# Optimization experiments

Measured on AMD Instinct MI355X. Metric: run time of the kernel, lower is better.

The kernel has to match this reference:

```python
import jax, jax.numpy as jnp
import numpy as np
from jax import lax

N_NODES = 20000
N_EDGES = 320000
FEAT = 100
N_RULES = 64
T_RULE = 50
H_RNN = 256
RULE_NUMS = 16
NTN_OUT = 200


def setup_inputs() -> dict:
    key = jax.random.key(0)
    ks = iter(jax.random.split(key, 64))
    nrm = lambda shape, s=0.05: jax.random.normal(next(ks), shape, jnp.float32) * s
    inp = {}
    inp["node_features_0"] = jax.random.normal(next(ks), (N_NODES, FEAT), jnp.float32)
    inp["node_features_1"] = jax.random.normal(next(ks), (N_NODES, FEAT), jnp.float32)
    inp["edge_indices_0"] = jax.random.randint(next(ks), (2, N_EDGES), 0, N_NODES)
    inp["edge_indices_1"] = jax.random.randint(next(ks), (2, N_EDGES), 0, N_NODES)
    inp["edge_features_0"] = jax.random.normal(next(ks), (N_EDGES, FEAT), jnp.float32)
    inp["edge_features_1"] = jax.random.normal(next(ks), (N_EDGES, FEAT), jnp.float32)
    inp["rules"] = jax.random.normal(next(ks), (N_RULES, T_RULE, FEAT), jnp.float32)
    # TripleConv 1: edge lin (3*100 -> 100) and nn = mlp (100->100->100)
    inp["c1_lin_W"] = nrm((FEAT, 3 * FEAT)); inp["c1_lin_b"] = jnp.zeros((FEAT,))
    inp["c1_W1"] = nrm((FEAT, FEAT)); inp["c1_b1"] = jnp.zeros((FEAT,))
    inp["c1_W2"] = nrm((FEAT, FEAT)); inp["c1_b2"] = jnp.zeros((FEAT,))
    # TripleConv 2
    inp["c2_lin_W"] = nrm((FEAT, 3 * FEAT)); inp["c2_lin_b"] = jnp.zeros((FEAT,))
    inp["c2_W1"] = nrm((FEAT, FEAT)); inp["c2_b1"] = jnp.zeros((FEAT,))
    inp["c2_W2"] = nrm((FEAT, FEAT)); inp["c2_b2"] = jnp.zeros((FEAT,))
    # NTN (input_dim=100 to match pooled graph vectors, out_dim=200)
    inp["ntn_W"] = nrm((FEAT, FEAT, NTN_OUT))
    inp["ntn_V"] = nrm((NTN_OUT, 2 * FEAT))
    inp["ntn_B"] = jnp.zeros((NTN_OUT,))
    # RuleEmbedding: 2-layer tanh RNN (100 -> 256 -> 256) + Linear(256,100)
    inp["rnn0_Wih"] = nrm((H_RNN, FEAT)); inp["rnn0_Whh"] = nrm((H_RNN, H_RNN))
    inp["rnn0_bih"] = jnp.zeros((H_RNN,)); inp["rnn0_bhh"] = jnp.zeros((H_RNN,))
    inp["rnn1_Wih"] = nrm((H_RNN, H_RNN)); inp["rnn1_Whh"] = nrm((H_RNN, H_RNN))
    inp["rnn1_bih"] = jnp.zeros((H_RNN,)); inp["rnn1_bhh"] = jnp.zeros((H_RNN,))
    inp["rule_lin_W"] = nrm((FEAT, H_RNN)); inp["rule_lin_b"] = jnp.zeros((FEAT,))
    # RuleRanker 100->128->64->1
    inp["rk_W1"] = nrm((128, FEAT)); inp["rk_b1"] = jnp.zeros((128,))
    inp["rk_W2"] = nrm((64, 128)); inp["rk_b2"] = jnp.zeros((64,))
    inp["rk_W3"] = nrm((1, 64)); inp["rk_b3"] = jnp.zeros((1,))
    # Head: fc1 (200 + rule_nums*100 -> 500) -> fc2 (500->100) -> fc3 (100->1)
    inp["fc1_W"] = nrm((500, NTN_OUT + RULE_NUMS * FEAT)); inp["fc1_b"] = jnp.zeros((500,))
    inp["fc2_W"] = nrm((FEAT, 500)); inp["fc2_b"] = jnp.zeros((FEAT,))
    inp["fc3_W"] = nrm((1, FEAT)); inp["fc3_b"] = jnp.zeros((1,))
    return inp


def _triple_conv(x, src, dst, e, lin_W, lin_b, W1, b1, W2, b2):
    # message: relu(Linear(concat(x_i, edge_attr, x_j))); PyG: i=target, j=source
    m = jax.nn.relu(jnp.concatenate([x[dst], e, x[src]], axis=1) @ lin_W.T + lin_b)
    agg = jax.ops.segment_sum(m, dst, num_segments=x.shape[0])  # aggr='add'
    out = agg + x  # (1 + eps) * x_r with eps = 0
    h = jax.nn.relu(out @ W1.T + b1)
    return h @ W2.T + b2  # nn = Sequential(Linear, ReLU, Linear)


def _conv_pass(x, ei, e, c_lin_W, c_lin_b, c_W1, c_b1, c_W2, c_b2,
               d_lin_W, d_lin_b, d_W1, d_b1, d_W2, d_b2):
    src, dst = ei[0], ei[1]
    x = jax.nn.relu(_triple_conv(x, src, dst, e, c_lin_W, c_lin_b, c_W1, c_b1, c_W2, c_b2))
    x = jax.nn.relu(_triple_conv(x, src, dst, e, d_lin_W, d_lin_b, d_W1, d_b1, d_W2, d_b2))
    return x


def _rnn_layer(x_tbf, Wih, Whh, bih, bhh):
    # x_tbf: [T, B, in]; returns all hidden states [T, B, H] and final [B, H]
    h0 = jnp.zeros((x_tbf.shape[1], Whh.shape[0]), x_tbf.dtype)
    def step(h, xt):
        h = jnp.tanh(xt @ Wih.T + bih + h @ Whh.T + bhh)
        return h, h
    hT, ys = lax.scan(step, h0, x_tbf)
    return ys, hT


def reference(node_features_0, node_features_1, edge_indices_0, edge_indices_1,
              edge_features_0, edge_features_1, rules,
              c1_lin_W, c1_lin_b, c1_W1, c1_b1, c1_W2, c1_b2,
              c2_lin_W, c2_lin_b, c2_W1, c2_b1, c2_W2, c2_b2,
              ntn_W, ntn_V, ntn_B,
              rnn0_Wih, rnn0_Whh, rnn0_bih, rnn0_bhh,
              rnn1_Wih, rnn1_Whh, rnn1_bih, rnn1_bhh,
              rule_lin_W, rule_lin_b,
              rk_W1, rk_b1, rk_W2, rk_b2, rk_W3, rk_b3,
              fc1_W, fc1_b, fc2_W, fc2_b, fc3_W, fc3_b):
    # --- rule embedding (all sequences full length => pack/pad is identity) ---
    x = jnp.transpose(rules, (1, 0, 2))  # [T, B, 100]
    ys, _ = _rnn_layer(x, rnn0_Wih, rnn0_Whh, rnn0_bih, rnn0_bhh)
    _, hT = _rnn_layer(ys, rnn1_Wih, rnn1_Whh, rnn1_bih, rnn1_bhh)
    rules_embedding = hT @ rule_lin_W.T + rule_lin_b  # [B, 100]
    # --- rule ranking + top-k ---
    h = jax.nn.relu(rules_embedding @ rk_W1.T + rk_b1)
    h = jax.nn.relu(h @ rk_W2.T + rk_b2)
    rules_score = jax.nn.sigmoid(h @ rk_W3.T + rk_b3)[:, 0]  # [B]
    _, top_idx = lax.top_k(rules_score, RULE_NUMS)
    top_rules_embedding = rules_embedding[top_idx]  # [rule_nums, 100]
    # --- GNN message passing on both graphs ---
    f1 = _conv_pass(node_features_0, edge_indices_0, edge_features_0,
                    c1_lin_W, c1_lin_b, c1_W1, c1_b1, c1_W2, c1_b2,
                    c2_lin_W, c2_lin_b, c2_W1, c2_b1, c2_W2, c2_b2)
    f2 = _conv_pass(node_features_1, edge_indices_1, edge_features_1,
                    c1_lin_W, c1_lin_b, c1_W1, c1_b1, c1_W2, c1_b2,
                    c2_lin_W, c2_lin_b, c2_W1, c2_b1, c2_W2, c2_b2)
    g1 = jnp.sum(f1, axis=0, keepdims=True)  # global_add_pool, single graph -> [1, 100]
    g2 = jnp.sum(f2, axis=0, keepdims=True)
    # --- NTN(g1, g2) ---
    tp = jnp.einsum('ai,ijk,bj->abk', g1, ntn_W, g2)  # [1,1,200]
    concat = jnp.concatenate([g1[:, None, :] * jnp.ones_like(g2)[None, :, :1],
                              g2[None, :, :] * jnp.ones_like(g1)[:, None, :1]], axis=2)
    lin_term = concat @ ntn_V.T  # [1,1,200]
    ntn_out = jax.nn.relu(tp + lin_term + ntn_B).reshape(-1)  # squeeze -> [200]
    # --- scoring head ---
    feat = jnp.concatenate([ntn_out, top_rules_embedding.reshape(-1)])  # [200 + rule_nums*100]
    z = jax.nn.relu(feat @ fc1_W.T + fc1_b)
    z = jax.nn.relu(z @ fc2_W.T + fc2_b)
    score = jax.nn.sigmoid(z @ fc3_W.T + fc3_b)
    return score.reshape(())
```

## Files before the change

### kernel.cpp

```cpp
#include <hip/hip_runtime.h>

typedef unsigned short u16;
typedef unsigned int u32;

#define N_NODES 20000
#define N_EDGES 320000
#define FEAT 100
#define XPAD 112
#define MPAD 104
#define N_RULES 64
#define T_RULE 50
#define H_RNN 256
#define RULE_NUMS 16
#define NTN_OUT 200
#define SCAN_B 79

typedef __attribute__((ext_vector_type(8))) short short8;
typedef __attribute__((ext_vector_type(4))) float f32x4;

__device__ __forceinline__ u16 f2bu(float f) {
  u32 u = __float_as_uint(f);
  u32 r = (u + 0x7fffu + ((u >> 16) & 1u)) >> 16;
  return (u16)r;
}
__device__ __forceinline__ float bu2f(u16 u) {
  return __uint_as_float(((u32)u) << 16);
}
__device__ __forceinline__ u32 pk2(float a, float b) {
  return (u32)f2bu(a) | ((u32)f2bu(b) << 16);
}

__device__ __forceinline__ void lds_st16(void* base, int byteOff, uint4 v) {
  *(uint4*)((char*)base + byteOff) = v;
}
__device__ __forceinline__ short8 lds_ld16(const void* base, int byteOff) {
  return *(const short8*)((const char*)base + byteOff);
}

#define SWZ(row, kByte) (((((row) << 8) + (kByte))) ^ (((row) & 7) << 4))

__device__ __forceinline__ int hs_off(int row, int chunk) {
  return (row << 9) | (((chunk + row * 5) & 31) << 4);
}

__device__ __forceinline__ float tanh_fast(float x) {
  const float e = __expf(2.f * x);
  return 1.f - 2.f / (e + 1.f);
}

__global__ void k_prep(const float* __restrict__ nf0, const float* __restrict__ nf1,
                       u16* __restrict__ xb0, u16* __restrict__ xb1) {
  const int total = N_NODES * XPAD;
  for (int i = blockIdx.x * blockDim.x + threadIdx.x; i < total;
       i += gridDim.x * blockDim.x) {
    const int n = i / XPAD;
    const int c = i - n * XPAD;
    const float v0 = (c < FEAT) ? nf0[(size_t)n * FEAT + c] : 0.f;
    const float v1 = (c < FEAT) ? nf1[(size_t)n * FEAT + c] : 0.f;
    xb0[i] = f2bu(v0);
    xb1[i] = f2bu(v1);
  }
}

__global__ void k_wprep(const float* __restrict__ linW, u16* __restrict__ Wb) {
  const int idx = blockIdx.x * blockDim.x + threadIdx.x;
  if (idx >= 3 * 128 * 128) return;
  const int c = idx >> 14;
  const int rem = idx & 16383;
  const int r = rem >> 7;
  const int k = rem & 127;
  u16 v = 0;
  if (r < FEAT && k < FEAT) v = f2bu(linW[(size_t)r * 300 + c * 100 + k]);
  Wb[idx] = v;
}

__global__ void k_wprep_sq(const float* __restrict__ W, u16* __restrict__ Wb) {
  const int idx = blockIdx.x * blockDim.x + threadIdx.x;
  if (idx >= 128 * 128) return;
  const int r = idx >> 7;
  const int k = idx & 127;
  u16 v = 0;
  if (r < FEAT && k < FEAT) v = f2bu(W[(size_t)r * FEAT + k]);
  Wb[idx] = v;
}

__global__ void k_count2(const int* __restrict__ d0, const int* __restrict__ d1,
                         int* __restrict__ cnt) {
  const int e = blockIdx.x * blockDim.x + threadIdx.x;
  const int* d = blockIdx.y ? d1 : d0;
  if (e < N_EDGES) atomicAdd(&cnt[blockIdx.y * N_NODES + d[e]], 1);
}

__global__ __launch_bounds__(256) void k_scan1(const int* __restrict__ cnt,
                                               int* __restrict__ off,
                                               int* __restrict__ bsum) {
  __shared__ int buf[256];
  const int g = blockIdx.y, b = blockIdx.x, tid = threadIdx.x;
  const int i = b * 256 + tid;
  const int v = (i < N_NODES) ? cnt[g * N_NODES + i] : 0;
  buf[tid] = v;
  __syncthreads();
  for (int ofs = 1; ofs < 256; ofs <<= 1) {
    const int t = (tid >= ofs) ? buf[tid - ofs] : 0;
    __syncthreads();
    buf[tid] += t;
    __syncthreads();
  }
  if (i < N_NODES) off[g * (N_NODES + 1) + i] = buf[tid] - v;
  if (tid == 255) bsum[g * SCAN_B + b] = buf[255];
}

__global__ __launch_bounds__(128) void k_scan2(int* __restrict__ bsum) {
  __shared__ int s[128];
  const int g = blockIdx.y, tid = threadIdx.x;
  const int v = (tid < SCAN_B) ? bsum[g * SCAN_B + tid] : 0;
  s[tid] = v;
  __syncthreads();
  for (int ofs = 1; ofs < 128; ofs <<= 1) {
    const int t = (tid >= ofs) ? s[tid - ofs] : 0;
    __syncthreads();
    s[tid] += t;
    __syncthreads();
  }
  if (tid < SCAN_B) bsum[g * SCAN_B + tid] = s[tid] - v;
}

__global__ __launch_bounds__(256) void k_scan3(const int* __restrict__ bsum,
                                               int* __restrict__ off,
                                               int* __restrict__ cursor) {
  const int g = blockIdx.y, b = blockIdx.x, tid = threadIdx.x;
  const int i = b * 256 + tid;
  if (i < N_NODES) {
    const int o = off[g * (N_NODES + 1) + i] + bsum[g * SCAN_B + b];
    off[g * (N_NODES + 1) + i] = o;
    cursor[g * N_NODES + i] = o;
  }
  if (i == N_NODES) off[g * (N_NODES + 1) + N_NODES] = N_EDGES;
}

__global__ void k_scatter2(const int* __restrict__ d0, const int* __restrict__ d1,
                           int* __restrict__ cursor, int* __restrict__ rank0,
                           int* __restrict__ rank1) {
  const int e = blockIdx.x * blockDim.x + threadIdx.x;
  const int g = blockIdx.y;
  const int* d = g ? d1 : d0;
  if (e < N_EDGES) {
    const int pos = atomicAdd(&cursor[g * N_NODES + d[e]], 1);
    (g ? rank1 : rank0)[e] = pos;
  }
}

template <int VARIANT>
__global__ __launch_bounds__(256) void k_gemm_u(
    const float* __restrict__ Af, const u16* __restrict__ Ab,
    const float* __restrict__ W, const float* __restrict__ b0,
    const float* __restrict__ b1, float* __restrict__ Uout) {
  __shared__ __align__(16) u16 As[64 * 128];
  __shared__ __align__(16) u16 Bs[128 * 128];
  const int tid = threadIdx.x;
  const int lane = tid & 63;
  const int wv = tid >> 6;
  const int l15 = lane & 15;
  const int lhi = lane >> 4;
  const int mb = blockIdx.x * 64;
  const int nb = blockIdx.y * 128;
  const int rb = (wv >> 1) * 32;
  const int cb = (wv & 1) * 64;
  constexpr int KV = VARIANT ? 256 : 100;
  constexpr int NPH = VARIANT ? 2 : 1;

  f32x4 acc[2][4];
  const f32x4 z4 = {0.f, 0.f, 0.f, 0.f};
#pragma unroll
  for (int i = 0; i < 2; ++i)
#pragma unroll
    for (int j = 0; j < 4; ++j) acc[i][j] = z4;

  for (int kc = 0; kc < NPH; ++kc) {
    __syncthreads();
    {
      const int row = tid >> 2;
      const int k0 = (tid & 3) * 32;
      const int gm = mb + row;
      if (VARIANT == 0) {
        const int r = gm & 63;
        const int t = gm >> 6;
        const float* ar = Af + ((size_t)r * T_RULE + t) * FEAT;
#pragma unroll
        for (int c = 0; c < 4; ++c) {
          const int k = k0 + c * 8;
          uint4 v = {0u, 0u, 0u, 0u};
          if (k + 8 <= KV) {
            const float4 fa = *(const float4*)(ar + k);
            const float4 fb = *(const float4*)(ar + k + 4);
            v.x = pk2(fa.x, fa.y); v.y = pk2(fa.z, fa.w);
            v.z = pk2(fb.x, fb.y); v.w = pk2(fb.z, fb.w);
          } else if (k < KV) {
            const float4 fa = *(const float4*)(ar + k);
            v.x = pk2(fa.x, fa.y); v.y = pk2(fa.z, fa.w);
          }
          lds_st16(As, SWZ(row, k * 2), v);
        }
      } else {
        const uint4* ar = (const uint4*)(Ab + (size_t)gm * 256 + kc * 128 + k0);
#pragma unroll
        for (int c = 0; c < 4; ++c)
          lds_st16(As, SWZ(row, (k0 + c * 8) * 2), ar[c]);
      }
    }
    {
      const int row = tid >> 1;
      const int k0 = (tid & 1) * 64;
      const float* wr = W + (size_t)(nb + row) * KV;
#pragma unroll
      for (int c = 0; c < 8; ++c) {
        const int k = k0 + c * 8;
        const int kg = kc * 128 + k;
        uint4 v = {0u, 0u, 0u, 0u};
        if (kg + 8 <= KV) {
          const float4 fa = *(const float4*)(wr + kg);
          const float4 fb = *(const float4*)(wr + kg + 4);
          v.x = pk2(fa.x, fa.y); v.y = pk2(fa.z, fa.w);
          v.z = pk2(fb.x, fb.y); v.w = pk2(fb.z, fb.w);
        } else if (kg < KV) {
          const float4 fa = *(const float4*)(wr + kg);
          v.x = pk2(fa.x, fa.y); v.y = pk2(fa.z, fa.w);
        }
        lds_st16(Bs, SWZ(row, k * 2), v);
      }
    }
    __syncthreads();
#pragma unroll
    for (int s = 0; s < 4; ++s) {
      const int kByte = s * 64 + lhi * 16;
      short8 af[2], bfr[4];
#pragma unroll
      for (int i = 0; i < 2; ++i)
        af[i] = lds_ld16(As, SWZ(rb + i * 16 + l15, kByte));
#pragma unroll
      for (int j = 0; j < 4; ++j)
        bfr[j] = lds_ld16(Bs, SWZ(cb + j * 16 + l15, kByte));
#pragma unroll
      for (int i = 0; i < 2; ++i)
#pragma unroll
        for (int j = 0; j < 4; ++j)
          acc[i][j] = __builtin_amdgcn_mfma_f32_16x16x32_bf16(af[i], bfr[j],
                                                              acc[i][j], 0, 0, 0);
    }
  }
#pragma unroll
  for (int j = 0; j < 4; ++j) {
    const int col = nb + cb + j * 16 + l15;
    const float bias = b0[col] + b1[col];
#pragma unroll
    for (int i = 0; i < 2; ++i) {
      const int base_m = mb + rb + i * 16 + lhi * 4;
      const int t = base_m >> 6;
      const int r0 = base_m & 63;
      float4 st;
      st.x = acc[i][j][0] + bias; st.y = acc[i][j][1] + bias;
      st.z = acc[i][j][2] + bias; st.w = acc[i][j][3] + bias;
      *(float4*)(Uout + ((size_t)t * 256 + col) * 64 + r0) = st;
    }
  }
}

template <int WRITE_YS>
__global__ __launch_bounds__(512) void k_rec(
    const float* __restrict__ U, const float* __restrict__ Whh,
    u16* __restrict__ ys, float* __restrict__ hT) {
  __shared__ __align__(16) u16 Hs[16 * 256];
  const int tid = threadIdx.x;
  const int lane = tid & 63;
  const int wv = tid >> 6;
  const int cbase = wv * 32;
  const int ruleBase = blockIdx.x * 16;
  const int l15 = lane & 15;
  const int lhi = lane >> 4;

  short8 bf[2][8];
#pragma unroll
  for (int jt = 0; jt < 2; ++jt) {
    const int col = cbase + jt * 16 + l15;
    const float* wr = Whh + (size_t)col * 256;
#pragma unroll
    for (int s = 0; s < 8; ++s) {
      const int k0 = s * 32 + lhi * 8;
      const float4 fa = *(const float4*)(wr + k0);
      const float4 fb = *(const float4*)(wr + k0 + 4);
      uint4 v;
      v.x = pk2(fa.x, fa.y); v.y = pk2(fa.z, fa.w);
      v.z = pk2(fb.x, fb.y); v.w = pk2(fb.z, fb.w);
      bf[jt][s] = *(short8*)&v;
    }
  }
  for (int i = tid; i < 16 * 256 / 8; i += 512) {
    const uint4 z = {0u, 0u, 0u, 0u};
    ((uint4*)Hs)[i] = z;
  }
  __syncthreads();

  const int n0 = cbase + l15;
  const int n1 = cbase + 16 + l15;
  const int m0 = lhi * 4;
  float4 Ua0 = *(const float4*)(U + ((size_t)n0) * 64 + m0);
  float4 Ua1 = *(const float4*)(U + ((size_t)n1) * 64 + m0);

  const f32x4 z4 = {0.f, 0.f, 0.f, 0.f};
  float hv[2][4];
  for (int t = 0; t < T_RULE; ++t) {
    const int tn = (t + 1 < T_RULE) ? t + 1 : t;
    const float4 Ub0 = *(const float4*)(U + ((size_t)tn * 256 + n0) * 64 + m0);
    const float4 Ub1 = *(const float4*)(U + ((size_t)tn * 256 + n1) * 64 + m0);
    f32x4 acc[2] = {z4, z4};
#pragma unroll
    for (int s = 0; s < 8; ++s) {
      const short8 af = lds_ld16(Hs, hs_off(l15, s * 4 + lhi));
      acc[0] = __builtin_amdgcn_mfma_f32_16x16x32_bf16(af, bf[0][s], acc[0], 0, 0, 0);
      acc[1] = __builtin_amdgcn_mfma_f32_16x16x32_bf16(af, bf[1][s], acc[1], 0, 0, 0);
    }
    const float ua0[4] = {Ua0.x, Ua0.y, Ua0.z, Ua0.w};
    const float ua1[4] = {Ua1.x, Ua1.y, Ua1.z, Ua1.w};
#pragma unroll
    for (int q = 0; q < 4; ++q) {
      hv[0][q] = tanh_fast(ua0[q] + acc[0][q]);
      hv[1][q] = tanh_fast(ua1[q] + acc[1][q]);
    }
    __syncthreads();
#pragma unroll
    for (int jt = 0; jt < 2; ++jt) {
      const int n = cbase + jt * 16 + l15;
#pragma unroll
      for (int q = 0; q < 4; ++q) {
        const int m = lhi * 4 + q;
        const u16 hb = f2bu(hv[jt][q]);
        *(u16*)((char*)Hs + (hs_off(m, n >> 3) + ((n & 7) << 1))) = hb;
        if (WRITE_YS)
          ys[(((size_t)t * 64 + ruleBase + m) << 8) + n] = hb;
      }
    }
    Ua0 = Ub0; Ua1 = Ub1;
    __syncthreads();
  }
  if (!WRITE_YS) {
#pragma unroll
    for (int jt = 0; jt < 2; ++jt) {
      const int n = cbase + jt * 16 + l15;
#pragma unroll
      for (int q = 0; q < 4; ++q) {
        const int m = lhi * 4 + q;
        hT[((size_t)(ruleBase + m) << 8) + n] = hv[jt][q];
      }
    }
  }
}

__global__ __launch_bounds__(128) void k_rulelin(
    const float* __restrict__ hT, const float* __restrict__ rlW,
    const float* __restrict__ rlb, float* __restrict__ emb) {
  __shared__ __align__(16) float hs[H_RNN];
  const int b = blockIdx.x;
  const int tid = threadIdx.x;
  for (int i = tid; i < H_RNN / 4; i += 128)
    ((float4*)hs)[i] = ((const float4*)(hT + (size_t)b * H_RNN))[i];
  __syncthreads();
  if (tid < FEAT) {
    float acc = rlb[tid];
    const float4* w = (const float4*)(rlW + (size_t)tid * H_RNN);
    const float4* hv = (const float4*)hs;
#pragma unroll 8
    for (int k = 0; k < 64; ++k) {
      const float4 a = w[k], x = hv[k];
      acc += a.x * x.x + a.y * x.y + a.z * x.z + a.w * x.w;
    }
    emb[(size_t)b * FEAT + tid] = acc;
  }
}

__global__ __launch_bounds__(128) void k_ranker(
    const float* __restrict__ emb,
    const float* __restrict__ W1, const float* __restrict__ b1,
    const float* __restrict__ W2, const float* __restrict__ b2,
    const float* __restrict__ W3, const float* __restrict__ b3,
    float* __restrict__ scores) {
  __shared__ float eb[FEAT];
  __shared__ float h1s[128];
  __shared__ float h2s[64];
  const int r = blockIdx.x;
  const int tid = threadIdx.x;
  if (tid < FEAT) eb[tid] = emb[(size_t)r * FEAT + tid];
  __syncthreads();
  {
    float acc = b1[tid];
    const float* w = W1 + (size_t)tid * FEAT;
    for (int k = 0; k < FEAT; ++k) acc += w[k] * eb[k];
    h1s[tid] = acc > 0.f ? acc : 0.f;
  }
  __syncthreads();
  if (tid < 64) {
    float acc = b2[tid];
    const float* w = W2 + (size_t)tid * 128;
    for (int k = 0; k < 128; ++k) acc += w[k] * h1s[k];
    h2s[tid] = acc > 0.f ? acc : 0.f;
  }
  __syncthreads();
  if (tid == 0) {
    float acc = b3[0];
    for (int k = 0; k < 64; ++k) acc += W3[k] * h2s[k];
    scores[r] = acc;
  }
}

__global__ void k_topk(const float* __restrict__ scores, int* __restrict__ topidx) {
  if (threadIdx.x == 0 && blockIdx.x == 0) {
    float s[N_RULES];
    for (int i = 0; i < N_RULES; ++i) s[i] = scores[i];
    for (int t = 0; t < RULE_NUMS; ++t) {
      int best = 0;
      float bv = s[0];
      for (int i = 1; i < N_RULES; ++i)
        if (s[i] > bv) { bv = s[i]; best = i; }
      topidx[t] = best;
      s[best] = -1e30f;
    }
  }
}

__global__ __launch_bounds__(256) void k_nodegemm(
    const u16* __restrict__ xb, const u16* __restrict__ Wb,
    const float* __restrict__ linB, u16* __restrict__ P, u16* __restrict__ Q) {
  __shared__ __align__(16) u16 As[128 * 128];
  __shared__ __align__(16) u16 Bs[128 * 128];
  const int tid = threadIdx.x;
  const int lane = tid & 63;
  const int wv = tid >> 6;
  const int l15 = lane & 15;
  const int lhi = lane >> 4;
  const int n0 = blockIdx.x * 128;
  const int p = blockIdx.y;
  const int rStage = tid >> 1;
  const int hf = tid & 1;
  const int rb = (wv >> 1) * 64;
  const int cb = (wv & 1) * 64;

  {
    const int node = n0 + rStage;
    const bool ok = node < N_NODES;
    const uint4* xr = (const uint4*)(xb + (size_t)node * XPAD);
#pragma unroll
    for (int q = 0; q < 8; ++q) {
      const int cc = hf * 8 + q;
      uint4 v = {0u, 0u, 0u, 0u};
      if (ok && cc < 14) v = xr[cc];
      lds_st16(As, SWZ(rStage, cc * 16), v);
    }
  }
  {
    const uint4* wr = (const uint4*)(Wb + (size_t)(p ? 2 : 0) * 16384 +
                                     (size_t)rStage * 128);
#pragma unroll
    for (int q = 0; q < 8; ++q) {
      const int cc = hf * 8 + q;
      lds_st16(Bs, SWZ(rStage, cc * 16), wr[cc]);
    }
  }
  __syncthreads();

  f32x4 acc[4][4];
  const f32x4 z4 = {0.f, 0.f, 0.f, 0.f};
#pragma unroll
  for (int i = 0; i < 4; ++i)
#pragma unroll
    for (int j = 0; j < 4; ++j) acc[i][j] = z4;
#pragma unroll
  for (int s = 0; s < 4; ++s) {
    const int kByte = s * 64 + lhi * 16;
    short8 af[4], bfr[4];
#pragma unroll
    for (int i = 0; i < 4; ++i) {
      af[i] = lds_ld16(As, SWZ(rb + i * 16 + l15, kByte));
      bfr[i] = lds_ld16(Bs, SWZ(cb + i * 16 + l15, kByte));
    }
#pragma unroll
    for (int i = 0; i < 4; ++i)
#pragma unroll
      for (int j = 0; j < 4; ++j)
        acc[i][j] = __builtin_amdgcn_mfma_f32_16x16x32_bf16(af[i], bfr[j],
                                                            acc[i][j], 0, 0, 0);
  }
  u16* Out = p ? Q : P;
#pragma unroll
  for (int j = 0; j < 4; ++j) {
    const int col = cb + j * 16 + l15;
    if (col >= XPAD) continue;
    const bool valid = col < FEAT;
    const float bias = (valid && !p) ? linB[col] : 0.f;
#pragma unroll
    for (int i = 0; i < 4; ++i) {
      const int row0 = rb + i * 16 + lhi * 4;
#pragma unroll
      for (int q = 0; q < 4; ++q) {
        const int node = n0 + row0 + q;
        if (node < N_NODES)
          Out[(size_t)node * XPAD + col] = valid ? f2bu(acc[i][j][q] + bias) : (u16)0;
      }
    }
  }
}

__global__ __launch_bounds__(256) void k_msgE(
    const float* __restrict__ ef, const u16* __restrict__ Wb,
    const int* __restrict__ srcI, const int* __restrict__ dstI,
    const int* __restrict__ rank, const u16* __restrict__ Pb,
    const u16* __restrict__ Qb, u16* __restrict__ mOut) {
  __shared__ __align__(16) u16 As[64 * 128];
  __shared__ __align__(16) u16 Bs[128 * 128];
  const int tid = threadIdx.x;
  const int lane = tid & 63;
  const int wv = tid >> 6;
  const int l15 = lane & 15;
  const int lhi = lane >> 4;
  const int e0 = blockIdx.x * 64;

  const int rr = tid >> 2;
  const int t4 = tid & 3;
  const int ge = e0 + rr;
  const int dn = dstI[ge];
  const int sn = srcI[ge];
  const int rk = rank[ge];
  uint4 pv[4], qv[4];
#pragma unroll
  for (int c = 0; c < 4; ++c) {
    const int chunk = t4 * 4 + c;
    uint4 z = {0u, 0u, 0u, 0u};
    pv[c] = z; qv[c] = z;
    if (chunk < 14) {
      pv[c] = *(const uint4*)(Pb + (size_t)dn * XPAD + chunk * 8);
      qv[c] = *(const uint4*)(Qb + (size_t)sn * XPAD + chunk * 8);
    }
  }

  {
    const int row = tid >> 2;
    const int k0 = (tid & 3) * 32;
    const float* ar = ef + (size_t)(e0 + row) * FEAT;
#pragma unroll
    for (int c = 0; c < 4; ++c) {
      const int k = k0 + c * 8;
      uint4 v = {0u, 0u, 0u, 0u};
      if (k + 8 <= FEAT) {
        const float4 fa = *(const float4*)(ar + k);
        const float4 fb = *(const float4*)(ar + k + 4);
        v.x = pk2(fa.x, fa.y); v.y = pk2(fa.z, fa.w);
        v.z = pk2(fb.x, fb.y); v.w = pk2(fb.z, fb.w);
      } else if (k < FEAT) {
        const float4 fa = *(const float4*)(ar + k);
        v.x = pk2(fa.x, fa.y); v.y = pk2(fa.z, fa.w);
      }
      lds_st16(As, SWZ(row, k * 2), v);
    }
  }
  {
    const int row = tid >> 1;
    const int hf = tid & 1;
    const uint4* wr = (const uint4*)(Wb + 16384 + (size_t)row * 128);
#pragma unroll
    for (int q = 0; q < 8; ++q) {
      const int cc = hf * 8 + q;
      lds_st16(Bs, SWZ(row, cc * 16), wr[cc]);
    }
  }
  __syncthreads();

  const int rb = (wv >> 1) * 32;
  const int cb = (wv & 1) * 64;
  f32x4 acc[2][4];
  const f32x4 z4 = {0.f, 0.f, 0.f, 0.f};
#pragma unroll
  for (int i = 0; i < 2; ++i)
#pragma unroll
    for (int j = 0; j < 4; ++j) acc[i][j] = z4;
#pragma unroll
  for (int s = 0; s < 4; ++s) {
    const int kByte = s * 64 + lhi * 16;
    short8 af[2], bfr[4];
#pragma unroll
    for (int i = 0; i < 2; ++i)
      af[i] = lds_ld16(As, SWZ(rb + i * 16 + l15, kByte));
#pragma unroll
    for (int j = 0; j < 4; ++j)
      bfr[j] = lds_ld16(Bs, SWZ(cb + j * 16 + l15, kByte));
#pragma unroll
    for (int i = 0; i < 2; ++i)
#pragma unroll
      for (int j = 0; j < 4; ++j)
        acc[i][j] = __builtin_amdgcn_mfma_f32_16x16x32_bf16(af[i], bfr[j],
                                                            acc[i][j], 0, 0, 0);
  }
  __syncthreads();
#pragma unroll
  for (int i = 0; i < 2; ++i) {
#pragma unroll
    for (int j = 0; j < 4; ++j) {
      const int col = cb + j * 16 + l15;
#pragma unroll
      for (int q = 0; q < 4; ++q) {
        const int row = rb + i * 16 + lhi * 4 + q;
        *(u16*)((char*)As + (SWZ(row, col * 2))) = f2bu(acc[i][j][q]);
      }
    }
  }
  __syncthreads();
#pragma unroll
  for (int c = 0; c < 4; ++c) {
    const int chunk = t4 * 4 + c;
    if (chunk > 12) break;
    const short8 ev = lds_ld16(As, SWZ(rr, chunk * 16));
    const uint4 e4 = *(const uint4*)&ev;
    const uint4 p4 = pv[c];
    const uint4 q4 = qv[c];
    uint4 o;
    {
      float v0 = bu2f((u16)(e4.x & 0xffffu)) + bu2f((u16)(p4.x & 0xffffu)) +
                 bu2f((u16)(q4.x & 0xffffu));
      float v1 = bu2f((u16)(e4.x >> 16)) + bu2f((u16)(p4.x >> 16)) +
                 bu2f((u16)(q4.x >> 16));
      o.x = pk2(v0 > 0.f ? v0 : 0.f, v1 > 0.f ? v1 : 0.f);
      float v2 = bu2f((u16)(e4.y & 0xffffu)) + bu2f((u16)(p4.y & 0xffffu)) +
                 bu2f((u16)(q4.y & 0xffffu));
      float v3 = bu2f((u16)(e4.y >> 16)) + bu2f((u16)(p4.y >> 16)) +
                 bu2f((u16)(q4.y >> 16));
      o.y = pk2(v2 > 0.f ? v2 : 0.f, v3 > 0.f ? v3 : 0.f);
      float v4 = bu2f((u16)(e4.z & 0xffffu)) + bu2f((u16)(p4.z & 0xffffu)) +
                 bu2f((u16)(q4.z & 0xffffu));
      float v5 = bu2f((u16)(e4.z >> 16)) + bu2f((u16)(p4.z >> 16)) +
                 bu2f((u16)(q4.z >> 16));
      o.z = pk2(v4 > 0.f ? v4 : 0.f, v5 > 0.f ? v5 : 0.f);
      float v6 = bu2f((u16)(e4.w & 0xffffu)) + bu2f((u16)(p4.w & 0xffffu)) +
                 bu2f((u16)(q4.w & 0xffffu));
      float v7 = bu2f((u16)(e4.w >> 16)) + bu2f((u16)(p4.w >> 16)) +
                 bu2f((u16)(q4.w >> 16));
      o.w = pk2(v6 > 0.f ? v6 : 0.f, v7 > 0.f ? v7 : 0.f);
    }
    *(uint4*)(mOut + (size_t)rk * MPAD + chunk * 8) = o;
  }
}

__global__ __launch_bounds__(256) void k_agg(
    const u16* __restrict__ mPerm, const int* __restrict__ off,
    const u16* __restrict__ xb, u16* __restrict__ aggb) {
  const int tid = threadIdx.x;
  const int ln = tid >> 5;
  const int j = tid & 31;
  const int n = blockIdx.x * 8 + ln;
  if (j >= 28) return;
  u16* outp = aggb + (size_t)n * XPAD + j * 4;
  if (j >= 26) {
    uint2 z = {0u, 0u};
    *(uint2*)outp = z;
    return;
  }
  const int p0 = off[n], p1 = off[n + 1];
  float a0 = 0.f, a1 = 0.f, a2 = 0.f, a3 = 0.f;
  const u16* mp = mPerm + (size_t)j * 4;
  int p = p0;
  for (; p + 3 < p1; p += 4) {
    const uint2 u0 = *(const uint2*)(mp + (size_t)p * MPAD);
    const uint2 u1 = *(const uint2*)(mp + (size_t)(p + 1) * MPAD);
    const uint2 u2 = *(const uint2*)(mp + (size_t)(p + 2) * MPAD);
    const uint2 u3 = *(const uint2*)(mp + (size_t)(p + 3) * MPAD);
    a0 += bu2f((u16)(u0.x & 0xffffu)) + bu2f((u16)(u1.x & 0xffffu)) +
          bu2f((u16)(u2.x & 0xffffu)) + bu2f((u16)(u3.x & 0xffffu));
    a1 += bu2f((u16)(u0.x >> 16)) + bu2f((u16)(u1.x >> 16)) +
          bu2f((u16)(u2.x >> 16)) + bu2f((u16)(u3.x >> 16));
    a2 += bu2f((u16)(u0.y & 0xffffu)) + bu2f((u16)(u1.y & 0xffffu)) +
          bu2f((u16)(u2.y & 0xffffu)) + bu2f((u16)(u3.y & 0xffffu));
    a3 += bu2f((u16)(u0.y >> 16)) + bu2f((u16)(u1.y >> 16)) +
          bu2f((u16)(u2.y >> 16)) + bu2f((u16)(u3.y >> 16));
  }
  for (; p < p1; ++p) {
    const uint2 u0 = *(const uint2*)(mp + (size_t)p * MPAD);
    a0 += bu2f((u16)(u0.x & 0xffffu));
    a1 += bu2f((u16)(u0.x >> 16));
    a2 += bu2f((u16)(u0.y & 0xffffu));
    a3 += bu2f((u16)(u0.y >> 16));
  }
  const uint2 xv = *(const uint2*)(xb + (size_t)n * XPAD + j * 4);
  a0 += bu2f((u16)(xv.x & 0xffffu));
  a1 += bu2f((u16)(xv.x >> 16));
  a2 += bu2f((u16)(xv.y & 0xffffu));
  a3 += bu2f((u16)(xv.y >> 16));
  uint2 o;
  o.x = pk2(a0, a1);
  o.y = pk2(a2, a3);
  *(uint2*)outp = o;
}

__global__ __launch_bounds__(256) void k_mlp(
    const u16* __restrict__ aggb, const u16* __restrict__ W1b,
    const float* __restrict__ b1, const u16* __restrict__ W2b,
    const float* __restrict__ b2, u16* __restrict__ xbout) {
  __shared__ __align__(16) u16 As[128 * 128];
  __shared__ __align__(16) u16 Bs[128 * 128];
  const int tid = threadIdx.x;
  const int lane = tid & 63;
  const int wv = tid >> 6;
  const int l15 = lane & 15;
  const int lhi = lane >> 4;
  const int n0 = blockIdx.x * 128;
  const int rStage = tid >> 1;
  const int hf = tid & 1;
  const int rb = (wv >> 1) * 64;
  const int cb = (wv & 1) * 64;
  const f32x4 z4 = {0.f, 0.f, 0.f, 0.f};

  {
    const int node = n0 + rStage;
    const bool ok = node < N_NODES;
    const uint4* xr = (const uint4*)(aggb + (size_t)node * XPAD);
#pragma unroll
    for (int q = 0; q < 8; ++q) {
      const int cc = hf * 8 + q;
      uint4 v = {0u, 0u, 0u, 0u};
      if (ok && cc < 14) v = xr[cc];
      lds_st16(As, SWZ(rStage, cc * 16), v);
    }
  }
  {
    const uint4* wr = (const uint4*)(W1b + (size_t)rStage * 128);
#pragma unroll
    for (int q = 0; q < 8; ++q) {
      const int cc = hf * 8 + q;
      lds_st16(Bs, SWZ(rStage, cc * 16), wr[cc]);
    }
  }
  __syncthreads();

  f32x4 acc[4][4];
#pragma unroll
  for (int i = 0; i < 4; ++i)
#pragma unroll
    for (int j = 0; j < 4; ++j) acc[i][j] = z4;
#pragma unroll
  for (int s = 0; s < 4; ++s) {
    const int kByte = s * 64 + lhi * 16;
    short8 af[4], bfr[4];
#pragma unroll
    for (int i = 0; i < 4; ++i) {
      af[i] = lds_ld16(As, SWZ(rb + i * 16 + l15, kByte));
      bfr[i] = lds_ld16(Bs, SWZ(cb + i * 16 + l15, kByte));
    }
#pragma unroll
    for (int i = 0; i < 4; ++i)
#pragma unroll
      for (int j = 0; j < 4; ++j)
        acc[i][j] = __builtin_amdgcn_mfma_f32_16x16x32_bf16(af[i], bfr[j],
                                                            acc[i][j], 0, 0, 0);
  }
  __syncthreads();
#pragma unroll
  for (int j = 0; j < 4; ++j) {
    const int col = cb + j * 16 + l15;
    const float bias = (col < FEAT) ? b1[col] : 0.f;
#pragma unroll
    for (int i = 0; i < 4; ++i) {
      const int row0 = rb + i * 16 + lhi * 4;
#pragma unroll
      for (int q = 0; q < 4; ++q) {
        float v = acc[i][j][q] + bias;
        v = v > 0.f ? v : 0.f;
        *(u16*)((char*)As + (SWZ(row0 + q, col * 2))) = f2bu(v);
      }
    }
  }
  {
    const uint4* wr = (const uint4*)(W2b + (size_t)rStage * 128);
#pragma unroll
    for (int q = 0; q < 8; ++q) {
      const int cc = hf * 8 + q;
      lds_st16(Bs, SWZ(rStage, cc * 16), wr[cc]);
    }
  }
  __syncthreads();

#pragma unroll
  for (int i = 0; i < 4; ++i)
#pragma unroll
    for (int j = 0; j < 4; ++j) acc[i][j] = z4;
#pragma unroll
  for (int s = 0; s < 4; ++s) {
    const int kByte = s * 64 + lhi * 16;
    short8 af[4], bfr[4];
#pragma unroll
    for (int i = 0; i < 4; ++i) {
      af[i] = lds_ld16(As, SWZ(rb + i * 16 + l15, kByte));
      bfr[i] = lds_ld16(Bs, SWZ(cb + i * 16 + l15, kByte));
    }
#pragma unroll
    for (int i = 0; i < 4; ++i)
#pragma unroll
      for (int j = 0; j < 4; ++j)
        acc[i][j] = __builtin_amdgcn_mfma_f32_16x16x32_bf16(af[i], bfr[j],
                                                            acc[i][j], 0, 0, 0);
  }
#pragma unroll
  for (int j = 0; j < 4; ++j) {
    const int col = cb + j * 16 + l15;
    if (col >= XPAD) continue;
    const bool valid = col < FEAT;
    const float bias = valid ? b2[col] : 0.f;
#pragma unroll
    for (int i = 0; i < 4; ++i) {
      const int row0 = rb + i * 16 + lhi * 4;
#pragma unroll
      for (int q = 0; q < 4; ++q) {
        const int node = n0 + row0 + q;
        if (node < N_NODES) {
          float v = acc[i][j][q] + bias;
          v = v > 0.f ? v : 0.f;
          xbout[(size_t)node * XPAD + col] = valid ? f2bu(v) : (u16)0;
        }
      }
    }
  }
}

__global__ void k_pool(const u16* __restrict__ xb, float* __restrict__ g) {
  const int tid = threadIdx.x;
  if (tid >= FEAT) return;
  float s = 0.f;
  const int n0 = blockIdx.x * 100;
  for (int i = 0; i < 100; ++i) s += bu2f(xb[(size_t)(n0 + i) * XPAD + tid]);
  atomicAdd(&g[tid], s);
}

__global__ __launch_bounds__(256) void k_ntn(const float* __restrict__ W,
                                             const float* __restrict__ g1,
                                             const float* __restrict__ g2,
                                             float* __restrict__ tp) {
  __shared__ float g2s[FEAT];
  const int i = blockIdx.x;
  const int tid = threadIdx.x;
  if (tid < FEAT) g2s[tid] = g2[tid];
  __syncthreads();
  if (tid < NTN_OUT) {
    const float g1i = g1[i];
    float acc = 0.f;
    const float* wr = W + (size_t)i * FEAT * NTN_OUT + tid;
    for (int jj = 0; jj < FEAT; ++jj) acc += wr[(size_t)jj * NTN_OUT] * g2s[jj];
    atomicAdd(&tp[tid], g1i * acc);
  }
}

__global__ __launch_bounds__(256) void k_feat(
    const float* __restrict__ tp, const float* __restrict__ gv,
    const float* __restrict__ V, const float* __restrict__ B,
    const float* __restrict__ emb, const int* __restrict__ topidx,
    float* __restrict__ featOut) {
  const int tid = threadIdx.x;
  if (tid < NTN_OUT) {
    float acc = B[tid] + tp[tid];
    const float* vr = V + (size_t)tid * 200;
    for (int k = 0; k < 200; ++k) acc += vr[k] * gv[k];
    featOut[tid] = acc > 0.f ? acc : 0.f;
  }
  for (int i = tid; i < RULE_NUMS * FEAT; i += 256) {
    const int rr = i / FEAT;
    const int cc = i - rr * FEAT;
    featOut[NTN_OUT + i] = emb[(size_t)topidx[rr] * FEAT + cc];
  }
}

__global__ __launch_bounds__(256) void k_fc1(
    const float* __restrict__ feat, const float* __restrict__ W,
    const float* __restrict__ b, float* __restrict__ z1) {
  __shared__ __align__(16) float fs[NTN_OUT + RULE_NUMS * FEAT];
  const int tid = threadIdx.x;
  for (int i = tid; i < 450; i += 256) ((float4*)fs)[i] = ((const float4*)feat)[i];
  __syncthreads();
  const int lane = tid & 63;
  const int wv = tid >> 6;
  const int o = blockIdx.x * 4 + wv;
  float acc = 0.f;
  const float4* w4 = (const float4*)(W + (size_t)o * 1800);
  const float4* f4 = (const float4*)fs;
  for (int k = lane; k < 450; k += 64) {
    const float4 a = w4[k], x = f4[k];
    acc += a.x * x.x + a.y * x.y + a.z * x.z + a.w * x.w;
  }
#pragma unroll
  for (int d = 32; d; d >>= 1) acc += __shfl_down(acc, d);
  if (lane == 0) {
    acc += b[o];
    z1[o] = acc > 0.f ? acc : 0.f;
  }
}

__global__ __launch_bounds__(128) void k_head2(
    const float* __restrict__ z1g, const float* __restrict__ fc2W,
    const float* __restrict__ fc2b, const float* __restrict__ fc3W,
    const float* __restrict__ fc3b, float* __restrict__ out) {
  __shared__ __align__(16) float z1[500];
  __shared__ float z2[FEAT];
  const int tid = threadIdx.x;
  for (int i = tid; i < 125; i += 128) ((float4*)z1)[i] = ((const float4*)z1g)[i];
  __syncthreads();
  if (tid < FEAT) {
    float acc = fc2b[tid];
    const float4* w4 = (const float4*)(fc2W + (size_t)tid * 500);
    const float4* f4 = (const float4*)z1;
#pragma unroll 5
    for (int k = 0; k < 125; ++k) {
      const float4 a = w4[k], x = f4[k];
      acc += a.x * x.x + a.y * x.y + a.z * x.z + a.w * x.w;
    }
    z2[tid] = acc > 0.f ? acc : 0.f;
  }
  __syncthreads();
  if (tid == 0) {
    float acc = fc3b[0];
    for (int k = 0; k < FEAT; ++k) acc += fc3W[k] * z2[k];
    out[0] = 1.f / (1.f + expf(-acc));
  }
}

extern "C" void kernel_launch(void* const* d_in, const int* in_sizes, int n_in,
                              void* d_out, int out_size, void* d_ws, size_t ws_size,
                              hipStream_t stream) {
  (void)in_sizes; (void)n_in; (void)out_size; (void)ws_size;

  const float* nf[2] = {(const float*)d_in[0], (const float*)d_in[1]};
  const int* ei[2] = {(const int*)d_in[2], (const int*)d_in[3]};
  const float* ef[2] = {(const float*)d_in[4], (const float*)d_in[5]};
  const float* rules = (const float*)d_in[6];
  const float* cw[2][6];
  for (int l = 0; l < 2; ++l)
    for (int k = 0; k < 6; ++k) cw[l][k] = (const float*)d_in[7 + l * 6 + k];
  const float* ntnW = (const float*)d_in[19];
  const float* ntnV = (const float*)d_in[20];
  const float* ntnB = (const float*)d_in[21];
  const float* r0Wih = (const float*)d_in[22];
  const float* r0Whh = (const float*)d_in[23];
  const float* r0bih = (const float*)d_in[24];
  const float* r0bhh = (const float*)d_in[25];
  const float* r1Wih = (const float*)d_in[26];
  const float* r1Whh = (const float*)d_in[27];
  const float* r1bih = (const float*)d_in[28];
  const float* r1bhh = (const float*)d_in[29];
  const float* rlW = (const float*)d_in[30];
  const float* rlb = (const float*)d_in[31];
  const float* rkW1 = (const float*)d_in[32];
  const float* rkb1 = (const float*)d_in[33];
  const float* rkW2 = (const float*)d_in[34];
  const float* rkb2 = (const float*)d_in[35];
  const float* rkW3 = (const float*)d_in[36];
  const float* rkb3 = (const float*)d_in[37];
  const float* fc1W = (const float*)d_in[38];
  const float* fc1b = (const float*)d_in[39];
  const float* fc2W = (const float*)d_in[40];
  const float* fc2b = (const float*)d_in[41];
  const float* fc3W = (const float*)d_in[42];
  const float* fc3b = (const float*)d_in[43];

  char* base = (char*)d_ws;
  size_t woff = 0;
#define WS_ALLOC(T, NAME, BYTES) \
  T* NAME = (T*)(base + woff);   \
  woff = (woff + (size_t)(BYTES) + 255) & ~(size_t)255;
  WS_ALLOC(u16, m_buf, (size_t)N_EDGES * MPAD * 2)
  WS_ALLOC(u16, xb0, (size_t)N_NODES * XPAD * 2)
  WS_ALLOC(u16, xb1, (size_t)N_NODES * XPAD * 2)
  WS_ALLOC(u16, Pbuf, (size_t)N_NODES * XPAD * 2)
  WS_ALLOC(u16, Qbuf, (size_t)N_NODES * XPAD * 2)
  WS_ALLOC(u16, aggb, (size_t)N_NODES * XPAD * 2)
  WS_ALLOC(u16, Wb0, (size_t)3 * 128 * 128 * 2)
  WS_ALLOC(u16, Wb1, (size_t)3 * 128 * 128 * 2)
  WS_ALLOC(u16, Wm, (size_t)4 * 128 * 128 * 2)
  WS_ALLOC(int, offAll, (size_t)2 * (N_NODES + 1) * 4)
  WS_ALLOC(int, cursor, (size_t)2 * N_NODES * 4)
  WS_ALLOC(int, bsum, (size_t)2 * SCAN_B * 4)
  WS_ALLOC(int, rank0, (size_t)N_EDGES * 4)
  WS_ALLOC(int, rank1, (size_t)N_EDGES * 4)
  WS_ALLOC(float, emb, (size_t)N_RULES * FEAT * 4)
  WS_ALLOC(float, scores, (size_t)N_RULES * 4)
  WS_ALLOC(int, topidx, (size_t)RULE_NUMS * 4)
  WS_ALLOC(float, gtp, (size_t)(2 * FEAT + NTN_OUT) * 4)
#undef WS_ALLOC
  u16* xb[2] = {xb0, xb1};
  int* rankg[2] = {rank0, rank1};
  u16* Wbl[2] = {Wb0, Wb1};
  float* gv = gtp;
  float* tp = gtp + 200;

  float* U   = (float*)m_buf;
  u16*   ys  = (u16*)((char*)m_buf + 3276800);
  float* hT  = (float*)((char*)m_buf + 4915200);
  float* featWS = (float*)((char*)m_buf + 4980736);
  float* z1WS   = (float*)((char*)m_buf + 4988160);

  hipMemsetAsync(cursor, 0, (size_t)2 * N_NODES * 4, stream);
  hipMemsetAsync(gtp, 0, (size_t)(2 * FEAT + NTN_OUT) * 4, stream);

  k_prep<<<2048, 256, 0, stream>>>(nf[0], nf[1], xb[0], xb[1]);
  k_wprep<<<192, 256, 0, stream>>>(cw[0][0], Wb0);
  k_wprep<<<192, 256, 0, stream>>>(cw[1][0], Wb1);
  k_wprep_sq<<<64, 256, 0, stream>>>(cw[0][2], Wm);
  k_wprep_sq<<<64, 256, 0, stream>>>(cw[0][4], Wm + 16384);
  k_wprep_sq<<<64, 256, 0, stream>>>(cw[1][2], Wm + 2 * 16384);
  k_wprep_sq<<<64, 256, 0, stream>>>(cw[1][4], Wm + 3 * 16384);

  const int* src0 = ei[0];
  const int* src1 = ei[1];
  const int* dst0 = ei[0] + N_EDGES;
  const int* dst1 = ei[1] + N_EDGES;
  k_count2<<<dim3(1250, 2), 256, 0, stream>>>(dst0, dst1, cursor);
  k_scan1<<<dim3(SCAN_B, 2), 256, 0, stream>>>(cursor, offAll, bsum);
  k_scan2<<<dim3(1, 2), 128, 0, stream>>>(bsum);
  k_scan3<<<dim3(SCAN_B, 2), 256, 0, stream>>>(bsum, offAll, cursor);
  k_scatter2<<<dim3(1250, 2), 256, 0, stream>>>(dst0, dst1, cursor, rank0, rank1);

  {
    dim3 gg(50, 2);
    k_gemm_u<0><<<gg, 256, 0, stream>>>(rules, nullptr, r0Wih, r0bih, r0bhh, U);
    k_rec<1><<<4, 512, 0, stream>>>(U, r0Whh, ys, nullptr);
    k_gemm_u<1><<<gg, 256, 0, stream>>>(nullptr, ys, r1Wih, r1bih, r1bhh, U);
    k_rec<0><<<4, 512, 0, stream>>>(U, r1Whh, nullptr, hT);
    k_rulelin<<<N_RULES, 128, 0, stream>>>(hT, rlW, rlb, emb);
  }
  k_ranker<<<N_RULES, 128, 0, stream>>>(emb, rkW1, rkb1, rkW2, rkb2, rkW3, rkb3,
                                        scores);
  k_topk<<<1, 64, 0, stream>>>(scores, topidx);

  for (int g = 0; g < 2; ++g) {
    const int* srcp = ei[g];
    const int* dstp = ei[g] + N_EDGES;
    const int* offg = offAll + g * (N_NODES + 1);
    for (int l = 0; l < 2; ++l) {
      k_nodegemm<<<dim3(157, 2), 256, 0, stream>>>(xb[g], Wbl[l], cw[l][1],
                                                   Pbuf, Qbuf);
      k_msgE<<<5000, 256, 0, stream>>>(ef[g], Wbl[l], srcp, dstp, rankg[g],
                                       Pbuf, Qbuf, m_buf);
      k_agg<<<2500, 256, 0, stream>>>(m_buf, offg, xb[g], aggb);
      k_mlp<<<157, 256, 0, stream>>>(aggb, Wm + (size_t)(2 * l) * 16384, cw[l][3],
                                     Wm + (size_t)(2 * l + 1) * 16384, cw[l][5],
                                     xb[g]);
    }
    k_pool<<<200, 128, 0, stream>>>(xb[g], gv + g * FEAT);
  }

  k_ntn<<<FEAT, 256, 0, stream>>>(ntnW, gv, gv + FEAT, tp);
  k_feat<<<1, 256, 0, stream>>>(tp, gv, ntnV, ntnB, emb, topidx, featWS);
  k_fc1<<<125, 256, 0, stream>>>(featWS, fc1W, fc1b, z1WS);
  k_head2<<<1, 128, 0, stream>>>(z1WS, fc2W, fc2b, fc3W, fc3b, (float*)d_out);
}
```

Measured before the change: 877.6 us.

## Hold edge-message weights in registers and shrink LDS in k_msgE

The edge-message kernel no longer stages the 128x128 weight tile in shared memory. Each wave now loads its own 32-column slice of B fragments straight from global memory into registers and computes all 64 rows of the tile, so LDS per block drops to the A tile alone. The kernel also gains a launch-bounds hint asking for 4 blocks per CU. The gathers of the destination and source node projections (P and Q) move from the kernel prologue into the epilogue, which lowers register pressure but exposes their latency after the MFMA phase. Separately, two host pointer variables that are no longer used are removed.

```diff
diff --git a/kernel.cpp b/kernel.cpp
--- a/kernel.cpp
+++ b/kernel.cpp
@@ -508,42 +508,40 @@
   }
 }
 
-__global__ __launch_bounds__(256) void k_msgE(
+__global__ __launch_bounds__(256, 4) void k_msgE(
     const float* __restrict__ ef, const u16* __restrict__ Wb,
     const int* __restrict__ srcI, const int* __restrict__ dstI,
     const int* __restrict__ rank, const u16* __restrict__ Pb,
     const u16* __restrict__ Qb, u16* __restrict__ mOut) {
   __shared__ __align__(16) u16 As[64 * 128];
-  __shared__ __align__(16) u16 Bs[128 * 128];
   const int tid = threadIdx.x;
   const int lane = tid & 63;
   const int wv = tid >> 6;
   const int l15 = lane & 15;
   const int lhi = lane >> 4;
   const int e0 = blockIdx.x * 64;
-
   const int rr = tid >> 2;
   const int t4 = tid & 3;
   const int ge = e0 + rr;
   const int dn = dstI[ge];
   const int sn = srcI[ge];
   const int rk = rank[ge];
-  uint4 pv[4], qv[4];
-#pragma unroll
-  for (int c = 0; c < 4; ++c) {
-    const int chunk = t4 * 4 + c;
-    uint4 z = {0u, 0u, 0u, 0u};
-    pv[c] = z; qv[c] = z;
-    if (chunk < 14) {
-      pv[c] = *(const uint4*)(Pb + (size_t)dn * XPAD + chunk * 8);
-      qv[c] = *(const uint4*)(Qb + (size_t)sn * XPAD + chunk * 8);
-    }
-  }
-
+  const int cb = wv * 32;
+
+  short8 bf[2][4];
   {
-    const int row = tid >> 2;
-    const int k0 = (tid & 3) * 32;
-    const float* ar = ef + (size_t)(e0 + row) * FEAT;
+    const u16* wbase = Wb + 16384;
+#pragma unroll
+    for (int jt = 0; jt < 2; ++jt) {
+      const u16* wr = wbase + (size_t)(cb + jt * 16 + l15) * 128;
+#pragma unroll
+      for (int s = 0; s < 4; ++s)
+        bf[jt][s] = *(const short8*)(wr + s * 32 + lhi * 8);
+    }
+  }
+  {
+    const int k0 = t4 * 32;
+    const float* ar = ef + (size_t)ge * FEAT;
 #pragma unroll
     for (int c = 0; c < 4; ++c) {
       const int k = k0 + c * 8;
@@ -557,55 +555,40 @@
         const float4 fa = *(const float4*)(ar + k);
         v.x = pk2(fa.x, fa.y); v.y = pk2(fa.z, fa.w);
       }
-      lds_st16(As, SWZ(row, k * 2), v);
-    }
-  }
-  {
-    const int row = tid >> 1;
-    const int hf = tid & 1;
-    const uint4* wr = (const uint4*)(Wb + 16384 + (size_t)row * 128);
-#pragma unroll
-    for (int q = 0; q < 8; ++q) {
-      const int cc = hf * 8 + q;
-      lds_st16(Bs, SWZ(row, cc * 16), wr[cc]);
-    }
-  }
-  __syncthreads();
-
-  const int rb = (wv >> 1) * 32;
-  const int cb = (wv & 1) * 64;
-  f32x4 acc[2][4];
+      lds_st16(As, SWZ(rr, k * 2), v);
+    }
+  }
+  __syncthreads();
+
+  f32x4 acc[4][2];
   const f32x4 z4 = {0.f, 0.f, 0.f, 0.f};
 #pragma unroll
-  for (int i = 0; i < 2; ++i)
-#pragma unroll
-    for (int j = 0; j < 4; ++j) acc[i][j] = z4;
+  for (int i = 0; i < 4; ++i)
+#pragma unroll
+    for (int j = 0; j < 2; ++j) acc[i][j] = z4;
 #pragma unroll
   for (int s = 0; s < 4; ++s) {
     const int kByte = s * 64 + lhi * 16;
-    short8 af[2], bfr[4];
-#pragma unroll
-    for (int i = 0; i < 2; ++i)
-      af[i] = lds_ld16(As, SWZ(rb + i * 16 + l15, kByte));
-#pragma unroll
-    for (int j = 0; j < 4; ++j)
-      bfr[j] = lds_ld16(Bs, SWZ(cb + j * 16 + l15, kByte));
-#pragma unroll
-    for (int i = 0; i < 2; ++i)
-#pragma unroll
-      for (int j = 0; j < 4; ++j)
-        acc[i][j] = __builtin_amdgcn_mfma_f32_16x16x32_bf16(af[i], bfr[j],
+    short8 af[4];
+#pragma unroll
+    for (int i = 0; i < 4; ++i)
+      af[i] = lds_ld16(As, SWZ(i * 16 + l15, kByte));
+#pragma unroll
+    for (int i = 0; i < 4; ++i)
+#pragma unroll
+      for (int j = 0; j < 2; ++j)
+        acc[i][j] = __builtin_amdgcn_mfma_f32_16x16x32_bf16(af[i], bf[j][s],
                                                             acc[i][j], 0, 0, 0);
   }
   __syncthreads();
 #pragma unroll
-  for (int i = 0; i < 2; ++i) {
-#pragma unroll
-    for (int j = 0; j < 4; ++j) {
+  for (int i = 0; i < 4; ++i) {
+#pragma unroll
+    for (int j = 0; j < 2; ++j) {
       const int col = cb + j * 16 + l15;
 #pragma unroll
       for (int q = 0; q < 4; ++q) {
-        const int row = rb + i * 16 + lhi * 4 + q;
+        const int row = i * 16 + lhi * 4 + q;
         *(u16*)((char*)As + (SWZ(row, col * 2))) = f2bu(acc[i][j][q]);
       }
     }
@@ -615,33 +598,31 @@
   for (int c = 0; c < 4; ++c) {
     const int chunk = t4 * 4 + c;
     if (chunk > 12) break;
+    const uint4 p4 = *(const uint4*)(Pb + (size_t)dn * XPAD + chunk * 8);
+    const uint4 q4 = *(const uint4*)(Qb + (size_t)sn * XPAD + chunk * 8);
     const short8 ev = lds_ld16(As, SWZ(rr, chunk * 16));
     const uint4 e4 = *(const uint4*)&ev;
-    const uint4 p4 = pv[c];
-    const uint4 q4 = qv[c];
     uint4 o;
-    {
-      float v0 = bu2f((u16)(e4.x & 0xffffu)) + bu2f((u16)(p4.x & 0xffffu)) +
-                 bu2f((u16)(q4.x & 0xffffu));
-      float v1 = bu2f((u16)(e4.x >> 16)) + bu2f((u16)(p4.x >> 16)) +
-                 bu2f((u16)(q4.x >> 16));
-      o.x = pk2(v0 > 0.f ? v0 : 0.f, v1 > 0.f ? v1 : 0.f);
-      float v2 = bu2f((u16)(e4.y & 0xffffu)) + bu2f((u16)(p4.y & 0xffffu)) +
-                 bu2f((u16)(q4.y & 0xffffu));
-      float v3 = bu2f((u16)(e4.y >> 16)) + bu2f((u16)(p4.y >> 16)) +
-                 bu2f((u16)(q4.y >> 16));
-      o.y = pk2(v2 > 0.f ? v2 : 0.f, v3 > 0.f ? v3 : 0.f);
-      float v4 = bu2f((u16)(e4.z & 0xffffu)) + bu2f((u16)(p4.z & 0xffffu)) +
-                 bu2f((u16)(q4.z & 0xffffu));
-      float v5 = bu2f((u16)(e4.z >> 16)) + bu2f((u16)(p4.z >> 16)) +
-                 bu2f((u16)(q4.z >> 16));
-      o.z = pk2(v4 > 0.f ? v4 : 0.f, v5 > 0.f ? v5 : 0.f);
-      float v6 = bu2f((u16)(e4.w & 0xffffu)) + bu2f((u16)(p4.w & 0xffffu)) +
-                 bu2f((u16)(q4.w & 0xffffu));
-      float v7 = bu2f((u16)(e4.w >> 16)) + bu2f((u16)(p4.w >> 16)) +
-                 bu2f((u16)(q4.w >> 16));
-      o.w = pk2(v6 > 0.f ? v6 : 0.f, v7 > 0.f ? v7 : 0.f);
-    }
+    float v0 = bu2f((u16)(e4.x & 0xffffu)) + bu2f((u16)(p4.x & 0xffffu)) +
+               bu2f((u16)(q4.x & 0xffffu));
+    float v1 = bu2f((u16)(e4.x >> 16)) + bu2f((u16)(p4.x >> 16)) +
+               bu2f((u16)(q4.x >> 16));
+    o.x = pk2(v0 > 0.f ? v0 : 0.f, v1 > 0.f ? v1 : 0.f);
+    float v2 = bu2f((u16)(e4.y & 0xffffu)) + bu2f((u16)(p4.y & 0xffffu)) +
+               bu2f((u16)(q4.y & 0xffffu));
+    float v3 = bu2f((u16)(e4.y >> 16)) + bu2f((u16)(p4.y >> 16)) +
+               bu2f((u16)(q4.y >> 16));
+    o.y = pk2(v2 > 0.f ? v2 : 0.f, v3 > 0.f ? v3 : 0.f);
+    float v4 = bu2f((u16)(e4.z & 0xffffu)) + bu2f((u16)(p4.z & 0xffffu)) +
+               bu2f((u16)(q4.z & 0xffffu));
+    float v5 = bu2f((u16)(e4.z >> 16)) + bu2f((u16)(p4.z >> 16)) +
+               bu2f((u16)(q4.z >> 16));
+    o.z = pk2(v4 > 0.f ? v4 : 0.f, v5 > 0.f ? v5 : 0.f);
+    float v6 = bu2f((u16)(e4.w & 0xffffu)) + bu2f((u16)(p4.w & 0xffffu)) +
+               bu2f((u16)(q4.w & 0xffffu));
+    float v7 = bu2f((u16)(e4.w >> 16)) + bu2f((u16)(p4.w >> 16)) +
+               bu2f((u16)(q4.w >> 16));
+    o.w = pk2(v6 > 0.f ? v6 : 0.f, v7 > 0.f ? v7 : 0.f);
     *(uint4*)(mOut + (size_t)rk * MPAD + chunk * 8) = o;
   }
 }
@@ -1009,8 +990,6 @@
   k_wprep_sq<<<64, 256, 0, stream>>>(cw[1][2], Wm + 2 * 16384);
   k_wprep_sq<<<64, 256, 0, stream>>>(cw[1][4], Wm + 3 * 16384);
 
-  const int* src0 = ei[0];
-  const int* src1 = ei[1];
   const int* dst0 = ei[0] + N_EDGES;
   const int* dst1 = ei[1] + N_EDGES;
   k_count2<<<dim3(1250, 2), 256, 0, stream>>>(dst0, dst1, cursor);
```

Measured after the change: 951.2 us, median of 3. 1.08x slower.
